# Optimization experiments

Hardware: AMD Instinct MI355X
Metric: run time of the kernel (lower is better)

The kernel has to match this reference:

```python
import jax, jax.numpy as jnp
import numpy as np

N_NODES = 50000
N_EDGES = 500000
IN_CH = 2
HID = 64
OUT_CH = 64
H1 = 4
H2 = 1
EDGE_DIM = 2


def _glorot(key, shape):
    fan_in, fan_out = shape[0], shape[1]
    lim = jnp.sqrt(6.0 / (fan_in + fan_out))
    return jax.random.uniform(key, shape, jnp.float32, -lim, lim)


def setup_inputs() -> dict:
    key = jax.random.key(0)
    ks = jax.random.split(key, 16)
    x = jax.random.uniform(ks[0], (N_NODES, IN_CH), jnp.float32)
    edge_index = jax.random.randint(ks[1], (2, N_EDGES), 0, N_NODES, dtype=jnp.int64)
    edge_attr = jax.random.uniform(ks[2], (N_EDGES, EDGE_DIM), jnp.float32)
    batch = jnp.zeros((N_NODES,), jnp.int32)
    # conv1 params (GATv2: lin_l, lin_r with bias, lin_edge no bias, att, out bias)
    W1l = _glorot(ks[3], (IN_CH, H1 * HID)); b1l = jnp.zeros((H1 * HID,), jnp.float32)
    W1r = _glorot(ks[4], (IN_CH, H1 * HID)); b1r = jnp.zeros((H1 * HID,), jnp.float32)
    W1e = _glorot(ks[5], (EDGE_DIM, H1 * HID))
    att1 = _glorot(ks[6], (H1, HID))
    bias1 = jnp.zeros((H1 * HID,), jnp.float32)
    # conv2 params
    W2l = _glorot(ks[7], (H1 * HID, H2 * OUT_CH)); b2l = jnp.zeros((H2 * OUT_CH,), jnp.float32)
    W2r = _glorot(ks[8], (H1 * HID, H2 * OUT_CH)); b2r = jnp.zeros((H2 * OUT_CH,), jnp.float32)
    W2e = _glorot(ks[9], (EDGE_DIM, H2 * OUT_CH))
    att2 = _glorot(ks[10], (H2, OUT_CH))
    bias2 = jnp.zeros((H2 * OUT_CH,), jnp.float32)
    return dict(x=x, edge_attr=edge_attr,
                W1l=W1l, b1l=b1l, W1r=W1r, b1r=b1r, W1e=W1e, att1=att1, bias1=bias1,
                W2l=W2l, b2l=b2l, W2r=W2r, b2r=b2r, W2e=W2e, att2=att2, bias2=bias2,
                edge_index=edge_index, batch=batch)


def _segment_softmax(alpha, seg, num_segments):
    # alpha: [E, H], seg: [E] destination ids
    amax = jax.ops.segment_max(alpha, seg, num_segments=num_segments)
    amax = jnp.where(jnp.isfinite(amax), amax, 0.0)
    ex = jnp.exp(alpha - amax[seg])
    denom = jax.ops.segment_sum(ex, seg, num_segments=num_segments)
    return ex / (denom[seg] + 1e-16)


def _gatv2_conv(x, edge_index, edge_attr, Wl, bl, Wr, br, We, att, bias, heads, out_c):
    N = x.shape[0]
    src, dst = edge_index[0], edge_index[1]
    # add self loops with fill_value='mean' for edge_attr (PyG default)
    ones = jnp.ones((src.shape[0],), x.dtype)
    deg = jax.ops.segment_sum(ones, dst, num_segments=N)
    loop_attr = jax.ops.segment_sum(edge_attr, dst, num_segments=N) / jnp.maximum(deg, 1.0)[:, None]
    loops = jnp.arange(N, dtype=src.dtype)
    src = jnp.concatenate([src, loops])
    dst = jnp.concatenate([dst, loops])
    ea = jnp.concatenate([edge_attr, loop_attr], axis=0)
    xl = (x @ Wl + bl).reshape(N, heads, out_c)   # source-side transform
    xr = (x @ Wr + br).reshape(N, heads, out_c)   # target-side transform
    ee = (ea @ We).reshape(-1, heads, out_c)
    e = jax.nn.leaky_relu(xl[src] + xr[dst] + ee, 0.2)   # [E', H, C]
    alpha = jnp.einsum('ehc,hc->eh', e, att)
    alpha = _segment_softmax(alpha, dst, N)
    out = jax.ops.segment_sum(xl[src] * alpha[..., None], dst, num_segments=N)
    return out.reshape(N, heads * out_c) + bias


def reference(x, edge_attr, W1l, b1l, W1r, b1r, W1e, att1, bias1,
              W2l, b2l, W2r, b2r, W2e, att2, bias2, edge_index, batch):
    h = jax.nn.elu(_gatv2_conv(x, edge_index, edge_attr, W1l, b1l, W1r, b1r, W1e, att1, bias1, H1, HID))
    # dropout skipped (eval mode)
    h = _gatv2_conv(h, edge_index, edge_attr, W2l, b2l, W2r, b2r, W2e, att2, bias2, H2, OUT_CH)
    # global_mean_pool over batch (single graph -> [1, OUT_CH])
    nb = 1
    cnt = jax.ops.segment_sum(jnp.ones((h.shape[0],), h.dtype), batch, num_segments=nb)
    pooled = jax.ops.segment_sum(h, batch, num_segments=nb) / jnp.maximum(cnt, 1.0)[:, None]
    return pooled
```

## Files before the change

### kernel.cpp

```cpp
#include <hip/hip_runtime.h>
#include <hip/hip_bf16.h>

#define N_NODES 50000
#define N_EDGES 500000
#define E_AUG   (N_EDGES + N_NODES)
#define NH1 4
#define HID 64
#define C2  64

#define NBUCK  196
#define BNODES 256
#define BCAP   4096

#define NL2B    2048
#define L2CHUNK 272
#define L2BINS  320

typedef unsigned int uint32;
typedef unsigned short ushort16;
typedef __attribute__((ext_vector_type(8))) short short8v;
typedef __attribute__((ext_vector_type(4))) float f32x4;

__device__ __forceinline__ ushort16 f2bf(float f) {
    union { float f; uint32 u; } v; v.f = f;
    uint32 u = v.u + (0x7FFFu + ((v.u >> 16) & 1u));
    return (ushort16)(u >> 16);
}
__device__ __forceinline__ float bf2f(ushort16 h) {
    union { uint32 u; float f; } v; v.u = ((uint32)h) << 16;
    return v.f;
}


__global__ void prep_kernel(const float* __restrict__ W1l, const float* __restrict__ b1l,
                            const float* __restrict__ W1r, const float* __restrict__ b1r,
                            const float* __restrict__ W1e, const float* __restrict__ att1,
                            const float* __restrict__ bias1,
                            const float* __restrict__ W2l, const float* __restrict__ W2r,
                            float* __restrict__ Wpack, float* __restrict__ Apack,
                            float4* __restrict__ wpk4, ushort16* __restrict__ Wt,
                            int* __restrict__ bcnt) {
    const int tid = threadIdx.x;
    int t = blockIdx.x * 256 + tid;
    if (blockIdx.x == 0) {
        bcnt[tid] = 0;
        {
            int h = tid >> 6, hc = tid;
            float* wp = &Wpack[((tid & 63) * 4 + h) * 8];
            wp[0] = W1l[hc];       wp[1] = W1l[256 + hc];
            wp[2] = W1r[hc];       wp[3] = W1r[256 + hc];
            wp[4] = W1e[hc];       wp[5] = W1e[256 + hc];
            wp[6] = b1l[hc] + b1r[hc];
            wp[7] = 0.4f * att1[hc];
            wpk4[hc] = make_float4(W1l[hc], W1l[256 + hc], b1l[hc] + bias1[hc], 0.0f);
        }
        if (tid < 28) {
            int h = tid / 7, comp = tid % 7;
            float s = 0.0f;
            for (int c = 0; c < 64; ++c) {
                int hc = h * 64 + c;
                float m;
                switch (comp) {
                    case 0: m = W1l[hc]; break;
                    case 1: m = W1l[256 + hc]; break;
                    case 2: m = W1r[hc]; break;
                    case 3: m = W1r[256 + hc]; break;
                    case 4: m = W1e[hc]; break;
                    case 5: m = W1e[256 + hc]; break;
                    default: m = b1l[hc] + b1r[hc]; break;
                }
                s += att1[hc] * m;
            }
            Apack[h * 8 + comp] = 0.6f * s;
        }
    }
    if (t < 128 * 256) {
        int c = t & 127, k = t >> 7;
        float w = (c < 64) ? W2l[k * 64 + c] : W2r[k * 64 + (c - 64)];
        Wt[c * 256 + k] = f2bf(w);
    }
}


#define HIST_BLOCKS ((N_EDGES / 2 + 255) / 256)

__global__ __launch_bounds__(256) void pass1_kernel(
    const int* __restrict__ ei, const float* __restrict__ ea,
    const float* __restrict__ x,
    const float* __restrict__ Wpack, const float* __restrict__ Apack,
    int4* __restrict__ st_meta, float4* __restrict__ st_alpha,
    int* __restrict__ bcnt) {
    __shared__ float sWp[2048];
    __shared__ float sA[32];
    __shared__ int lbc[NBUCK];
    __shared__ int lbase[NBUCK];
    const int tid = threadIdx.x;
    for (int i = tid; i < 2048; i += 256) sWp[i] = Wpack[i];
    if (tid < 32) sA[tid] = Apack[tid];
    if (tid < NBUCK) lbc[tid] = 0;
    __syncthreads();

    const int e0 = (blockIdx.x * 256 + tid) * 2;
    int4 rec[2]; int bket[2], lofs[2];
    bool val[2];
    float u0[2], u1[2], u2[2], u3[2], u4[2], u5[2];
    #pragma unroll
    for (int j = 0; j < 2; ++j) {
        const int e = e0 + j;
        val[j] = (e < N_EDGES);
        if (val[j]) {
            const int s = ei[e], d = ei[N_EDGES + e];
            const float2 a = *(const float2*)&ea[2 * e];
            rec[j].x = s; rec[j].y = d;
            rec[j].z = __float_as_int(a.x); rec[j].w = __float_as_int(a.y);
            bket[j] = d >> 8;
            lofs[j] = atomicAdd(&lbc[bket[j]], 1);
            const float2 xs = *(const float2*)&x[2 * s];
            const float2 xd = *(const float2*)&x[2 * d];
            u0[j] = xs.x; u1[j] = xs.y; u2[j] = xd.x; u3[j] = xd.y;
            u4[j] = a.x;  u5[j] = a.y;
        } else {
            u0[j] = u1[j] = u2[j] = u3[j] = u4[j] = u5[j] = 0.0f;
        }
    }

    float p[4][2];
    #pragma unroll
    for (int h = 0; h < 4; ++h) {
        const float a0 = sA[h * 8], a1 = sA[h * 8 + 1], a2 = sA[h * 8 + 2],
                    a3 = sA[h * 8 + 3], a4 = sA[h * 8 + 4], a5 = sA[h * 8 + 5],
                    a6 = sA[h * 8 + 6];
        #pragma unroll
        for (int j = 0; j < 2; ++j)
            p[h][j] = fmaf(u0[j], a0, fmaf(u1[j], a1, fmaf(u2[j], a2,
                      fmaf(u3[j], a3, fmaf(u4[j], a4, fmaf(u5[j], a5, a6))))));
    }
    for (int c = 0; c < 64; ++c) {
        const float* wp = &sWp[c * 32];
        #pragma unroll
        for (int h = 0; h < 4; ++h) {
            const float4 wa = *(const float4*)&wp[h * 8];
            const float4 wb = *(const float4*)&wp[h * 8 + 4];
            #pragma unroll
            for (int j = 0; j < 2; ++j) {
                float tt = fmaf(u0[j], wa.x, fmaf(u1[j], wa.y, fmaf(u2[j], wa.z,
                           fmaf(u3[j], wa.w, fmaf(u4[j], wb.x, fmaf(u5[j], wb.y, wb.z))))));
                p[h][j] = fmaf(fabsf(tt), wb.w, p[h][j]);
            }
        }
    }

    __syncthreads();
    if (tid < NBUCK) lbase[tid] = lbc[tid] ? atomicAdd(&bcnt[tid], lbc[tid]) : 0;
    __syncthreads();
    #pragma unroll
    for (int j = 0; j < 2; ++j)
        if (val[j]) {
            int pos = bket[j] * BCAP + lbase[bket[j]] + lofs[j];
            st_meta[pos] = rec[j];
            st_alpha[pos] = make_float4(__expf(p[0][j]), __expf(p[1][j]),
                                        __expf(p[2][j]), __expf(p[3][j]));
        }
}


__global__ void bscan_kernel(const int* __restrict__ bcnt, int* __restrict__ bbase,
                             int* __restrict__ offs) {
    __shared__ int s[256];
    int tid = threadIdx.x;
    int nodec = (tid < NBUCK) ? min(BNODES, N_NODES - tid * BNODES) : 0;
    int v = (tid < NBUCK) ? bcnt[tid] + nodec : 0;
    s[tid] = v;
    __syncthreads();
    for (int off = 1; off < 256; off <<= 1) {
        int t = (tid >= off) ? s[tid - off] : 0;
        __syncthreads();
        s[tid] += t;
        __syncthreads();
    }
    if (tid < NBUCK) bbase[tid] = s[tid] - v;
    if (tid == 0) offs[N_NODES] = E_AUG;
}


__global__ __launch_bounds__(256) void buildk_kernel(
    const int4* __restrict__ st_meta, const float4* __restrict__ st_alpha,
    const int* __restrict__ bcnt, const int* __restrict__ bbase,
    int* __restrict__ offs, float* __restrict__ den,
    int4* __restrict__ epk, int* __restrict__ e_src, float4* __restrict__ af) {
    __shared__ int bins[256];
    __shared__ float ls0[256], ls1[256];
    __shared__ int scan[256];
    __shared__ int cursor[256];
    const int tid = threadIdx.x, bk = blockIdx.x;
    bins[tid] = 0; ls0[tid] = 0.0f; ls1[tid] = 0.0f;
    __syncthreads();

    const int n_ = bcnt[bk];
    const int4* sb = st_meta + (size_t)bk * BCAP;
    const float4* sa = st_alpha + (size_t)bk * BCAP;
    for (int i = tid; i < n_; i += 256) {
        int4 r = sb[i];
        int li = r.y & 255;
        atomicAdd(&bins[li], 1);
        atomicAdd(&ls0[li], __int_as_float(r.z));
        atomicAdd(&ls1[li], __int_as_float(r.w));
    }
    __syncthreads();

    const int node = bk * BNODES + tid;
    const int v = (node < N_NODES) ? bins[tid] + 1 : 0;
    scan[tid] = v;
    __syncthreads();
    for (int off = 1; off < 256; off <<= 1) {
        int t = (tid >= off) ? scan[tid - off] : 0;
        __syncthreads();
        scan[tid] += t;
        __syncthreads();
    }
    const int o = bbase[bk] + scan[tid] - v;
    if (node < N_NODES) {
        offs[node] = o;
        den[node] = 0.0f;
        float dgf = (float)max(bins[tid], 1);
        int4 sl;
        sl.x = node; sl.y = node;
        sl.z = __float_as_int(ls0[tid] / dgf);
        sl.w = __float_as_int(ls1[tid] / dgf);
        epk[o] = sl;
        e_src[o] = node;
    }
    cursor[tid] = o + 1;
    __syncthreads();

    for (int i = tid; i < n_; i += 256) {
        int4 r = sb[i];
        int pos = atomicAdd(&cursor[r.y & 255], 1);
        epk[pos] = r;
        e_src[pos] = r.x;
        af[pos] = sa[i];
    }
}


__global__ __launch_bounds__(256) void l1out_fused_kernel(
    const float* __restrict__ x, const int* __restrict__ offs,
    const int* __restrict__ e_src, const float4* __restrict__ af,
    const int4* __restrict__ epk,
    const float* __restrict__ Wpack, const float* __restrict__ Apack,
    const float4* __restrict__ wpk4, const ushort16* __restrict__ Wt,
    const float* __restrict__ b2l, const float* __restrict__ b2r,
    ushort16* __restrict__ xl2b, ushort16* __restrict__ xr2b) {
    __shared__ short hlds[64 * 256];
    __shared__ float4 swpk[256];
    __shared__ float sWp[2048];
    __shared__ float sA[32];
    const int tid = threadIdx.x;
    const int n0 = blockIdx.x * 64;
    const int lane = tid & 63, w = tid >> 6;

    swpk[tid] = wpk4[tid];
    for (int i = tid; i < 2048; i += 256) sWp[i] = Wpack[i];
    if (tid < 32) sA[tid] = Apack[tid];
    __syncthreads();

    const int nl = tid >> 2, head = tid & 3;
    const int node = n0 + nl;
    float S1 = 0.0f, S2 = 0.0f;
    if (node < N_NODES) {
        const int beg = offs[node], end = offs[node + 1];
        const float2 xn = *(const float2*)&x[2 * node];
        const int4 se = epk[beg];
        const float u0 = xn.x, u1 = xn.y, u4 = __int_as_float(se.z), u5 = __int_as_float(se.w);
        float ps = fmaf(u0, sA[head * 8] + sA[head * 8 + 2],
                   fmaf(u1, sA[head * 8 + 1] + sA[head * 8 + 3],
                   fmaf(u4, sA[head * 8 + 4], fmaf(u5, sA[head * 8 + 5], sA[head * 8 + 6]))));
        for (int c = 0; c < 64; ++c) {
            const float* wp = &sWp[c * 32 + head * 8];
            const float4 wa = *(const float4*)wp;
            const float4 wb = *(const float4*)(wp + 4);
            float tt = fmaf(u0, wa.x + wa.z, fmaf(u1, wa.y + wa.w,
                       fmaf(u4, wb.x, fmaf(u5, wb.y, wb.z))));
            ps = fmaf(fabsf(tt), wb.w, ps);
        }
        float selfw = __expf(ps);
        float den = selfw, s1 = selfw * u0, s2 = selfw * u1;
        const float* afp = (const float*)af;
        for (int e = beg + 1; e < end; ++e) {
            float wt = afp[4 * e + head];
            int s = e_src[e];
            float2 xs = *(const float2*)&x[2 * s];
            den += wt;
            s1 = fmaf(wt, xs.x, s1);
            s2 = fmaf(wt, xs.y, s2);
        }
        float inv = 1.0f / (den + 1e-16f);
        S1 = s1 * inv;
        S2 = s2 * inv;
    }

    {
        const int kseg = head * 64;
        const int swz = (nl & 7) << 3;
        for (int i = 0; i < 8; ++i) {
            short8v hv;
            #pragma unroll
            for (int j = 0; j < 8; ++j) {
                float4 wv = swpk[kseg + i * 8 + j];
                float g = fmaf(wv.x, S1, fmaf(wv.y, S2, wv.z));
                g = g > 0.0f ? g : (__expf(g) - 1.0f);
                hv[j] = (short)f2bf(g);
            }
            *(short8v*)&hlds[(nl * 256 + kseg + i * 8) ^ swz] = hv;
        }
    }

    short8v bfrag[2][8];
    {
        const int bc = w * 32 + (lane & 15);
        const int k0 = (lane >> 4) * 8;
        #pragma unroll
        for (int ct = 0; ct < 2; ++ct)
            #pragma unroll
            for (int kb = 0; kb < 8; ++kb)
                bfrag[ct][kb] = *(const short8v*)&Wt[(size_t)(bc + ct * 16) * 256 + kb * 32 + k0];
    }
    __syncthreads();

    f32x4 acc[4][2];
    #pragma unroll
    for (int rt = 0; rt < 4; ++rt)
        #pragma unroll
        for (int ct = 0; ct < 2; ++ct)
            acc[rt][ct] = (f32x4){0.0f, 0.0f, 0.0f, 0.0f};

    const int arow = lane & 15, ak0 = (lane >> 4) * 8;
    #pragma unroll
    for (int rt = 0; rt < 4; ++rt) {
        const int n = rt * 16 + arow;
        const int swz = (n & 7) << 3;
        #pragma unroll
        for (int kb = 0; kb < 8; ++kb) {
            short8v a = *(const short8v*)&hlds[(n * 256 + kb * 32 + ak0) ^ swz];
            acc[rt][0] = __builtin_amdgcn_mfma_f32_16x16x32_bf16(a, bfrag[0][kb], acc[rt][0], 0, 0, 0);
            acc[rt][1] = __builtin_amdgcn_mfma_f32_16x16x32_bf16(a, bfrag[1][kb], acc[rt][1], 0, 0, 0);
        }
    }

    #pragma unroll
    for (int ct = 0; ct < 2; ++ct) {
        const int c = w * 32 + ct * 16 + (lane & 15);
        const bool isL = (c < 64);
        const int cc = isL ? c : c - 64;
        const float bias = isL ? b2l[cc] : b2r[cc];
        ushort16* dst = isL ? xl2b : xr2b;
        #pragma unroll
        for (int rt = 0; rt < 4; ++rt)
            #pragma unroll
            for (int r = 0; r < 4; ++r) {
                int nn = n0 + rt * 16 + (lane >> 4) * 4 + r;
                if (nn < N_NODES) dst[nn * 64 + cc] = f2bf(acc[rt][ct][r] + bias);
            }
    }
}


__global__ __launch_bounds__(256) void l2_logit_kernel(
    const ushort16* __restrict__ xl2b, const ushort16* __restrict__ xr2b,
    const int4* __restrict__ epk,
    const float* __restrict__ W2e, const float* __restrict__ att2,
    float* __restrict__ alpha2, float* __restrict__ den) {
    __shared__ float sWe[128], satt[64];
    __shared__ float bins[L2BINS];
    const int tid = threadIdx.x;
    if (tid < 128) sWe[tid] = W2e[tid];
    if (tid < 64) satt[tid] = att2[tid];
    for (int i = tid; i < L2BINS; i += 256) bins[i] = 0.0f;
    const int base = blockIdx.x * L2CHUNK;
    const int d_first = epk[min(base, E_AUG - 1)].y;
    __syncthreads();

    const int lane = tid & 63, w = tid >> 6;
    const int cl = lane & 15, g = lane >> 4;
    const uint32* xlp = (const uint32*)xl2b;
    const uint32* xrp = (const uint32*)xr2b;

    for (int it = 0; it < L2CHUNK / 16; ++it) {
        const int e = base + it * 16 + w * 4 + g;
        if (e < E_AUG) {
            const int4 v = epk[e];
            const float ae0 = __int_as_float(v.z), ae1 = __int_as_float(v.w);
            float acc = 0.0f;
            #pragma unroll
            for (int q = 0; q < 2; ++q) {
                const int c2 = cl + q * 16;
                const uint32 ul = xlp[v.x * 32 + c2];
                const uint32 ur = xrp[v.y * 32 + c2];
                const int c0 = 2 * c2, c1 = 2 * c2 + 1;
                float xl0 = bf2f((ushort16)(ul & 0xffff)), xl1 = bf2f((ushort16)(ul >> 16));
                float xr0 = bf2f((ushort16)(ur & 0xffff)), xr1 = bf2f((ushort16)(ur >> 16));
                float t0 = xl0 + xr0 + fmaf(ae0, sWe[c0], ae1 * sWe[64 + c0]);
                float t1 = xl1 + xr1 + fmaf(ae0, sWe[c1], ae1 * sWe[64 + c1]);
                t0 = t0 > 0.0f ? t0 : 0.2f * t0;
                t1 = t1 > 0.0f ? t1 : 0.2f * t1;
                acc = fmaf(t0, satt[c0], fmaf(t1, satt[c1], acc));
            }
            #pragma unroll
            for (int off = 8; off; off >>= 1) acc += __shfl_xor(acc, off);
            if (cl == 0) {
                float wv = __expf(acc);
                alpha2[e] = wv;
                int rel = v.y - d_first;
                if (rel < L2BINS) atomicAdd(&bins[rel], wv);
                else atomicAdd(&den[v.y], wv);
            }
        }
    }
    __syncthreads();
    for (int i = tid; i < L2BINS; i += 256) {
        float b = bins[i];
        int node = d_first + i;
        if (b != 0.0f && node < N_NODES) atomicAdd(&den[node], b);
    }
}


__global__ __launch_bounds__(256) void l2_pool_kernel(
    const ushort16* __restrict__ xl2b, const int4* __restrict__ epk,
    const float* __restrict__ alpha2, const float* __restrict__ den,
    float* __restrict__ pblock) {
    __shared__ float sp[16][64];
    const int tid = threadIdx.x;
    const int lane = tid & 63, w = tid >> 6;
    const int cl = lane & 15, g = lane >> 4;
    const int slot = w * 4 + g;
    const int base = blockIdx.x * L2CHUNK;
    const uint32* xlp = (const uint32*)xl2b;

    float a0 = 0.0f, a1 = 0.0f, a2 = 0.0f, a3 = 0.0f;
    for (int it = 0; it < L2CHUNK / 16; ++it) {
        const int e = base + it * 16 + w * 4 + g;
        if (e < E_AUG) {
            const int4 v = epk[e];
            const float coef = alpha2[e] / (den[v.y] + 1e-16f);
            const uint32 u0 = xlp[v.x * 32 + cl];
            const uint32 u1 = xlp[v.x * 32 + cl + 16];
            a0 = fmaf(coef, bf2f((ushort16)(u0 & 0xffff)), a0);
            a1 = fmaf(coef, bf2f((ushort16)(u0 >> 16)), a1);
            a2 = fmaf(coef, bf2f((ushort16)(u1 & 0xffff)), a2);
            a3 = fmaf(coef, bf2f((ushort16)(u1 >> 16)), a3);
        }
    }
    sp[slot][2 * cl] = a0;
    sp[slot][2 * cl + 1] = a1;
    sp[slot][2 * cl + 32] = a2;
    sp[slot][2 * cl + 33] = a3;
    __syncthreads();
    if (tid < 64) {
        float s = 0.0f;
        #pragma unroll
        for (int i = 0; i < 16; ++i) s += sp[i][tid];
        pblock[blockIdx.x * 64 + tid] = s;
    }
}


__global__ __launch_bounds__(256) void pool_partial_kernel(const float* __restrict__ pblock,
                                                           float* __restrict__ pfin) {
    __shared__ float s[256];
    int tid = threadIdx.x;
    int l = tid & 63, q = tid >> 6;
    float local = 0.0f;
    for (int r = blockIdx.x * 4 + q; r < NL2B; r += 64 * 4)
        local += pblock[r * 64 + l];
    s[tid] = local;
    __syncthreads();
    if (tid < 64) {
        float v = s[tid] + s[tid + 64] + s[tid + 128] + s[tid + 192];
        pfin[blockIdx.x * 64 + tid] = v;
    }
}

__global__ __launch_bounds__(256) void pool_final2_kernel(const float* __restrict__ pfin,
                                                          const float* __restrict__ bias2,
                                                          float* __restrict__ d_out) {
    __shared__ float s[256];
    int tid = threadIdx.x;
    int l = tid & 63, q = tid >> 6;
    float local = 0.0f;
    for (int r = q; r < 64; r += 4)
        local += pfin[r * 64 + l];
    s[tid] = local;
    __syncthreads();
    if (tid < 64) {
        float v = s[tid] + s[tid + 64] + s[tid + 128] + s[tid + 192];
        d_out[tid] = v * (1.0f / N_NODES) + bias2[tid];
    }
}


extern "C" void kernel_launch(void* const* d_in, const int* in_sizes, int n_in,
                              void* d_out, int out_size, void* d_ws, size_t ws_size,
                              hipStream_t stream) {
    const float* x     = (const float*)d_in[0];
    const float* eattr = (const float*)d_in[1];
    const float* W1l   = (const float*)d_in[2];
    const float* b1l   = (const float*)d_in[3];
    const float* W1r   = (const float*)d_in[4];
    const float* b1r   = (const float*)d_in[5];
    const float* W1e   = (const float*)d_in[6];
    const float* att1  = (const float*)d_in[7];
    const float* bias1 = (const float*)d_in[8];
    const float* W2l   = (const float*)d_in[9];
    const float* b2l   = (const float*)d_in[10];
    const float* W2r   = (const float*)d_in[11];
    const float* b2r   = (const float*)d_in[12];
    const float* W2e   = (const float*)d_in[13];
    const float* att2  = (const float*)d_in[14];
    const float* bias2 = (const float*)d_in[15];
    const int*   ei    = (const int*)d_in[16];
    float* out = (float*)d_out;

    char* p = (char*)d_ws;
    auto alloc = [&](size_t bytes) -> void* {
        void* r = (void*)p;
        p += (bytes + 255) & ~(size_t)255;
        return r;
    };
    int*   bcnt   = (int*)alloc(256 * 4);
    int*   bbase  = (int*)alloc(256 * 4);
    int*   offs   = (int*)alloc((N_NODES + 1) * 4);
    float* den    = (float*)alloc(N_NODES * 4);
    int4*  st_meta  = (int4*)alloc((size_t)NBUCK * BCAP * 16);
    float4* st_alpha = (float4*)alloc((size_t)NBUCK * BCAP * 16);
    int4*  epk    = (int4*)alloc((size_t)E_AUG * 16);
    int*   e_src  = (int*)alloc(E_AUG * 4);
    float4* af    = (float4*)alloc((size_t)E_AUG * 16);
    float* alpha2 = (float*)alloc((size_t)E_AUG * 4);
    float* Wpack  = (float*)alloc(256 * 8 * 4);
    float* Apack  = (float*)alloc(32 * 4);
    float4* wpk4  = (float4*)alloc(256 * 16);
    ushort16* Wt  = (ushort16*)alloc(128 * 256 * 2);
    ushort16* xl2b = (ushort16*)alloc((size_t)N_NODES * C2 * 2);
    ushort16* xr2b = (ushort16*)alloc((size_t)N_NODES * C2 * 2);
    float* pblock = (float*)alloc((size_t)NL2B * 64 * 4);
    float* pfin   = (float*)alloc((size_t)64 * 64 * 4);

    prep_kernel<<<128, 256, 0, stream>>>(W1l, b1l, W1r, b1r, W1e, att1, bias1, W2l, W2r,
                                         Wpack, Apack, wpk4, Wt, bcnt);

    pass1_kernel<<<HIST_BLOCKS, 256, 0, stream>>>(ei, eattr, x, Wpack, Apack,
                                                  st_meta, st_alpha, bcnt);

    bscan_kernel<<<1, 256, 0, stream>>>(bcnt, bbase, offs);

    buildk_kernel<<<NBUCK, 256, 0, stream>>>(st_meta, st_alpha, bcnt, bbase,
                                             offs, den, epk, e_src, af);

    l1out_fused_kernel<<<(N_NODES + 63) / 64, 256, 0, stream>>>(
        x, offs, e_src, af, epk, Wpack, Apack, wpk4, Wt, b2l, b2r, xl2b, xr2b);

    l2_logit_kernel<<<NL2B, 256, 0, stream>>>(xl2b, xr2b, epk, W2e, att2, alpha2, den);

    l2_pool_kernel<<<NL2B, 256, 0, stream>>>(xl2b, epk, alpha2, den, pblock);

    pool_partial_kernel<<<64, 256, 0, stream>>>(pblock, pfin);
    pool_final2_kernel<<<1, 256, 0, stream>>>(pfin, bias2, out);
}
```

Before: 181.2 us.

## Materialize source features per edge and move self-loop logit into CSR build

The pass1 kernel now stores each edge's source node features (x[src]) next to its staged record, and the CSR build kernel scatters them into a new per-edge xsrc array. The layer-1 aggregation then streams contiguous xsrc instead of doing an indirect e_src lookup followed by a gather from x. The self-loop attention weight, previously computed in l1out_fused, is now computed in buildk and written into af, which removes that 64-iteration loop and the Wpack/Apack shared-memory loads from the aggregation kernel. In exchange there are extra 8-byte writes and reads per edge, and the self-loop work runs in buildk, which has only 196 blocks and so has limited parallelism.

Result: no change. 180.3 us (-0.5%).

```diff
diff --git a/kernel.cpp b/kernel.cpp
--- a/kernel.cpp
+++ b/kernel.cpp
@@ -89,7 +89,7 @@
     const float* __restrict__ x,
     const float* __restrict__ Wpack, const float* __restrict__ Apack,
     int4* __restrict__ st_meta, float4* __restrict__ st_alpha,
-    int* __restrict__ bcnt) {
+    float2* __restrict__ st_x, int* __restrict__ bcnt) {
     __shared__ float sWp[2048];
     __shared__ float sA[32];
     __shared__ int lbc[NBUCK];
@@ -160,6 +160,7 @@
             st_meta[pos] = rec[j];
             st_alpha[pos] = make_float4(__expf(p[0][j]), __expf(p[1][j]),
                                         __expf(p[2][j]), __expf(p[3][j]));
+            st_x[pos] = make_float2(u0[j], u1[j]);
         }
 }
 
@@ -185,20 +186,29 @@
 
 __global__ __launch_bounds__(256) void buildk_kernel(
     const int4* __restrict__ st_meta, const float4* __restrict__ st_alpha,
+    const float2* __restrict__ st_x,
     const int* __restrict__ bcnt, const int* __restrict__ bbase,
+    const float* __restrict__ xg,
+    const float* __restrict__ Wpack, const float* __restrict__ Apack,
     int* __restrict__ offs, float* __restrict__ den,
-    int4* __restrict__ epk, int* __restrict__ e_src, float4* __restrict__ af) {
+    int4* __restrict__ epk, int* __restrict__ e_src,
+    float4* __restrict__ af, float2* __restrict__ xsrc) {
     __shared__ int bins[256];
     __shared__ float ls0[256], ls1[256];
     __shared__ int scan[256];
     __shared__ int cursor[256];
+    __shared__ float sWp[2048];
+    __shared__ float sA[32];
     const int tid = threadIdx.x, bk = blockIdx.x;
     bins[tid] = 0; ls0[tid] = 0.0f; ls1[tid] = 0.0f;
+    for (int i = tid; i < 2048; i += 256) sWp[i] = Wpack[i];
+    if (tid < 32) sA[tid] = Apack[tid];
     __syncthreads();
 
     const int n_ = bcnt[bk];
     const int4* sb = st_meta + (size_t)bk * BCAP;
     const float4* sa = st_alpha + (size_t)bk * BCAP;
+    const float2* sx = st_x + (size_t)bk * BCAP;
     for (int i = tid; i < n_; i += 256) {
         int4 r = sb[i];
         int li = r.y & 255;
@@ -223,12 +233,32 @@
         offs[node] = o;
         den[node] = 0.0f;
         float dgf = (float)max(bins[tid], 1);
+        float u4 = ls0[tid] / dgf, u5 = ls1[tid] / dgf;
         int4 sl;
         sl.x = node; sl.y = node;
-        sl.z = __float_as_int(ls0[tid] / dgf);
-        sl.w = __float_as_int(ls1[tid] / dgf);
+        sl.z = __float_as_int(u4); sl.w = __float_as_int(u5);
         epk[o] = sl;
         e_src[o] = node;
+        const float2 xn = *(const float2*)&xg[2 * node];
+        const float u0 = xn.x, u1 = xn.y;
+        float4 alf;
+        #pragma unroll
+        for (int h = 0; h < 4; ++h) {
+            float ps = fmaf(u0, sA[h * 8] + sA[h * 8 + 2],
+                       fmaf(u1, sA[h * 8 + 1] + sA[h * 8 + 3],
+                       fmaf(u4, sA[h * 8 + 4], fmaf(u5, sA[h * 8 + 5], sA[h * 8 + 6]))));
+            for (int c = 0; c < 64; ++c) {
+                const float* wp = &sWp[c * 32 + h * 8];
+                const float4 wa = *(const float4*)wp;
+                const float4 wb = *(const float4*)(wp + 4);
+                float tt = fmaf(u0, wa.x + wa.z, fmaf(u1, wa.y + wa.w,
+                           fmaf(u4, wb.x, fmaf(u5, wb.y, wb.z))));
+                ps = fmaf(fabsf(tt), wb.w, ps);
+            }
+            alf[h] = __expf(ps);
+        }
+        af[o] = *(float4*)&alf;
+        xsrc[o] = xn;
     }
     cursor[tid] = o + 1;
     __syncthreads();
@@ -239,57 +269,35 @@
         epk[pos] = r;
         e_src[pos] = r.x;
         af[pos] = sa[i];
+        xsrc[pos] = sx[i];
     }
 }
 
 
 __global__ __launch_bounds__(256) void l1out_fused_kernel(
-    const float* __restrict__ x, const int* __restrict__ offs,
-    const int* __restrict__ e_src, const float4* __restrict__ af,
-    const int4* __restrict__ epk,
-    const float* __restrict__ Wpack, const float* __restrict__ Apack,
+    const int* __restrict__ offs, const float4* __restrict__ af,
+    const float2* __restrict__ xsrc,
     const float4* __restrict__ wpk4, const ushort16* __restrict__ Wt,
     const float* __restrict__ b2l, const float* __restrict__ b2r,
     ushort16* __restrict__ xl2b, ushort16* __restrict__ xr2b) {
     __shared__ short hlds[64 * 256];
     __shared__ float4 swpk[256];
-    __shared__ float sWp[2048];
-    __shared__ float sA[32];
     const int tid = threadIdx.x;
     const int n0 = blockIdx.x * 64;
     const int lane = tid & 63, w = tid >> 6;
 
     swpk[tid] = wpk4[tid];
-    for (int i = tid; i < 2048; i += 256) sWp[i] = Wpack[i];
-    if (tid < 32) sA[tid] = Apack[tid];
-    __syncthreads();
 
     const int nl = tid >> 2, head = tid & 3;
     const int node = n0 + nl;
     float S1 = 0.0f, S2 = 0.0f;
     if (node < N_NODES) {
         const int beg = offs[node], end = offs[node + 1];
-        const float2 xn = *(const float2*)&x[2 * node];
-        const int4 se = epk[beg];
-        const float u0 = xn.x, u1 = xn.y, u4 = __int_as_float(se.z), u5 = __int_as_float(se.w);
-        float ps = fmaf(u0, sA[head * 8] + sA[head * 8 + 2],
-                   fmaf(u1, sA[head * 8 + 1] + sA[head * 8 + 3],
-                   fmaf(u4, sA[head * 8 + 4], fmaf(u5, sA[head * 8 + 5], sA[head * 8 + 6]))));
-        for (int c = 0; c < 64; ++c) {
-            const float* wp = &sWp[c * 32 + head * 8];
-            const float4 wa = *(const float4*)wp;
-            const float4 wb = *(const float4*)(wp + 4);
-            float tt = fmaf(u0, wa.x + wa.z, fmaf(u1, wa.y + wa.w,
-                       fmaf(u4, wb.x, fmaf(u5, wb.y, wb.z))));
-            ps = fmaf(fabsf(tt), wb.w, ps);
-        }
-        float selfw = __expf(ps);
-        float den = selfw, s1 = selfw * u0, s2 = selfw * u1;
         const float* afp = (const float*)af;
-        for (int e = beg + 1; e < end; ++e) {
+        float den = 0.0f, s1 = 0.0f, s2 = 0.0f;
+        for (int e = beg; e < end; ++e) {
             float wt = afp[4 * e + head];
-            int s = e_src[e];
-            float2 xs = *(const float2*)&x[2 * s];
+            float2 xs = xsrc[e];
             den += wt;
             s1 = fmaf(wt, xs.x, s1);
             s2 = fmaf(wt, xs.y, s2);
@@ -298,6 +306,7 @@
         S1 = s1 * inv;
         S2 = s2 * inv;
     }
+    __syncthreads();
 
     {
         const int kseg = head * 64;
@@ -533,9 +542,11 @@
     float* den    = (float*)alloc(N_NODES * 4);
     int4*  st_meta  = (int4*)alloc((size_t)NBUCK * BCAP * 16);
     float4* st_alpha = (float4*)alloc((size_t)NBUCK * BCAP * 16);
+    float2* st_x  = (float2*)alloc((size_t)NBUCK * BCAP * 8);
     int4*  epk    = (int4*)alloc((size_t)E_AUG * 16);
     int*   e_src  = (int*)alloc(E_AUG * 4);
     float4* af    = (float4*)alloc((size_t)E_AUG * 16);
+    float2* xsrc  = (float2*)alloc((size_t)E_AUG * 8);
     float* alpha2 = (float*)alloc((size_t)E_AUG * 4);
     float* Wpack  = (float*)alloc(256 * 8 * 4);
     float* Apack  = (float*)alloc(32 * 4);
@@ -550,15 +561,16 @@
                                          Wpack, Apack, wpk4, Wt, bcnt);
 
     pass1_kernel<<<HIST_BLOCKS, 256, 0, stream>>>(ei, eattr, x, Wpack, Apack,
-                                                  st_meta, st_alpha, bcnt);
+                                                  st_meta, st_alpha, st_x, bcnt);
 
     bscan_kernel<<<1, 256, 0, stream>>>(bcnt, bbase, offs);
 
-    buildk_kernel<<<NBUCK, 256, 0, stream>>>(st_meta, st_alpha, bcnt, bbase,
-                                             offs, den, epk, e_src, af);
+    buildk_kernel<<<NBUCK, 256, 0, stream>>>(st_meta, st_alpha, st_x, bcnt, bbase,
+                                             x, Wpack, Apack,
+                                             offs, den, epk, e_src, af, xsrc);
 
     l1out_fused_kernel<<<(N_NODES + 63) / 64, 256, 0, stream>>>(
-        x, offs, e_src, af, epk, Wpack, Apack, wpk4, Wt, b2l, b2r, xl2b, xr2b);
+        offs, af, xsrc, wpk4, Wt, b2l, b2r, xl2b, xr2b);
 
     l2_logit_kernel<<<NL2B, 256, 0, stream>>>(xl2b, xr2b, epk, W2e, att2, alpha2, den);
 
```
